# Kernel tuning notes

Hardware: AMD Instinct MI355X
Metric: run time of the kernel (lower is better)

Reference implementation:

```python
import jax, jax.numpy as jnp
import numpy as np

N = 100000
E = 1600000
F = 64
THETA = (0.6, -0.4, 0.3, -0.2, 0.1)  # k = 5 polynomial coefficients


def setup_inputs() -> dict:
    key = jax.random.key(0)
    kx, ke = jax.random.split(key)
    x = jax.random.normal(kx, (N, F), dtype=jnp.float32)
    edge_index = jax.random.randint(ke, (2, E), 0, N, dtype=jnp.int64)
    return {"x": x, "edge_index": edge_index}


def _l_sym_mul(feat, src, dst, deg_inv_sqrt, n):
    # L_sym * feat = feat - D^{-1/2} A D^{-1/2} feat
    src_norm = feat[src] * deg_inv_sqrt[src]            # [E, F] gather + scale
    agg = jax.ops.segment_sum(src_norm, dst, num_segments=n)  # scatter-add to dst
    return feat - deg_inv_sqrt * agg


def reference(x, edge_index):
    src, dst = edge_index[0], edge_index[1]
    n = x.shape[0]
    # in-degree from dst, clamp to >= 1, D^{-1/2} as [N, 1]
    deg = jax.ops.segment_sum(jnp.ones((src.shape[0],), dtype=x.dtype), dst,
                              num_segments=n)
    deg = jnp.maximum(deg, 1.0)[:, None]
    deg_inv_sqrt = deg ** -0.5

    h_acc = THETA[0] * x
    feat = x
    for k in range(1, len(THETA)):
        feat = _l_sym_mul(feat, src, dst, deg_inv_sqrt, n)
        h_acc = h_acc + THETA[k] * feat
    return h_acc
```

## Files before the change

### kernel.cpp

```cpp
#include <hip/hip_runtime.h>


constexpr int kF = 64;
constexpr int BSHIFT = 8;
constexpr int NB = 1 << BSHIFT;
constexpr int TILE = 2048;
constexpr int KMAX = 512;

static __device__ __forceinline__ float bfl(unsigned u) {
    return __uint_as_float(u << 16);
}
static __device__ __forceinline__ float bfh(unsigned u) {
    return __uint_as_float(u & 0xffff0000u);
}
static __device__ __forceinline__ unsigned f2bf(float f) {
    unsigned u = __float_as_uint(f);
    return (u + 0x7fffu + ((u >> 16) & 1u)) >> 16;
}
static __device__ __forceinline__ unsigned pack2(float a, float b) {
    return f2bf(a) | (f2bf(b) << 16);
}

__global__ void k_binA(const int* __restrict__ src, const int* __restrict__ dst,
                       unsigned* __restrict__ pairs, int* __restrict__ gcursor,
                       const float4* __restrict__ x4, uint4* __restrict__ xb4,
                       int n8, int E, int K, int cap) {
    __shared__ int hist[KMAX];
    __shared__ int gb[KMAX];
    const int tid = threadIdx.x;
    const long long tb = (long long)blockIdx.x * TILE;
    const int tcount = (int)min((long long)TILE, (long long)E - tb);

    {
        int per = (n8 + gridDim.x - 1) / (int)gridDim.x;
        int b0 = blockIdx.x * per;
        int b1 = min(b0 + per, n8);
        for (int i = b0 + tid; i < b1; i += 512) {
            float4 a = x4[2 * i];
            float4 b = x4[2 * i + 1];
            uint4 o;
            o.x = pack2(a.x, a.y);
            o.y = pack2(a.z, a.w);
            o.z = pack2(b.x, b.y);
            o.w = pack2(b.z, b.w);
            xb4[i] = o;
        }
    }

    hist[tid] = 0;
    __syncthreads();
    int dc[4], sc[4];
    #pragma unroll
    for (int k = 0; k < 4; ++k) {
        int i = tid + k * 512;
        if (i < tcount) {
            dc[k] = dst[tb + i];
            sc[k] = src[tb + i];
            atomicAdd(&hist[dc[k] >> BSHIFT], 1);
        } else {
            dc[k] = -1;
        }
    }
    __syncthreads();
    int hv = hist[tid];
    gb[tid] = (tid < K && hv > 0) ? atomicAdd(&gcursor[tid], hv) : 0;
    hist[tid] = 0;
    __syncthreads();
    #pragma unroll
    for (int k = 0; k < 4; ++k) {
        if (dc[k] >= 0) {
            int d = dc[k];
            int b = d >> BSHIFT;
            int pos = atomicAdd(&hist[b], 1);
            pairs[(size_t)b * cap + gb[b] + pos] =
                ((unsigned)(d & (NB - 1)) << 23) | (unsigned)sc[k];
        }
    }
}

__global__ void k_binB(const unsigned* __restrict__ pairs, const int* __restrict__ gcursor,
                       int* __restrict__ rp, float* __restrict__ dinv2,
                       float* __restrict__ rdeg, int* __restrict__ csr,
                       const uint4* __restrict__ xb, uint4* __restrict__ g0,
                       int N, int E, int K, int cap) {
    __shared__ int gsc[KMAX];
    __shared__ int cnt[NB];
    __shared__ int stmp[NB];
    __shared__ int cur[NB];
    __shared__ float sdinv[NB];
    const int b = blockIdx.x;
    const int tid = threadIdx.x;

    int gv = (tid < K) ? gcursor[tid] : 0;
    gsc[tid] = gv;
    __syncthreads();
    for (int o = 1; o < KMAX; o <<= 1) {
        int t = (tid >= o) ? gsc[tid - o] : 0;
        __syncthreads();
        gsc[tid] += t;
        __syncthreads();
    }
    const int ecnt = gcursor[b];
    const int base = gsc[b] - ecnt;
    const unsigned* bp = pairs + (size_t)b * cap;

    if (tid < NB) cnt[tid] = 0;
    __syncthreads();
    for (int i = tid; i < ecnt; i += 512)
        atomicAdd(&cnt[bp[i] >> 23], 1);
    __syncthreads();
    int v = (tid < NB) ? cnt[tid] : 0;
    if (tid < NB) stmp[tid] = v;
    __syncthreads();
    for (int o = 1; o < NB; o <<= 1) {
        int t = (tid >= o && tid < NB) ? stmp[tid - o] : 0;
        __syncthreads();
        if (tid < NB) stmp[tid] += t;
        __syncthreads();
    }
    int node = (b << BSHIFT) + tid;
    if (tid < NB) {
        int abs0 = base + stmp[tid] - v;
        cur[tid] = abs0;
        float d = fmaxf((float)v, 1.0f);
        sdinv[tid] = rsqrtf(d);
        if (node < N) {
            rp[node] = abs0;
            dinv2[node] = 1.0f / d;
            rdeg[node]  = sqrtf(d);
        }
    }
    if (b == K - 1 && tid == 0) rp[N] = E;
    __syncthreads();
    for (int i = tid; i < ecnt; i += 512) {
        unsigned p = bp[i];
        int pos = atomicAdd(&cur[p >> 23], 1);
        csr[pos] = (int)(p & 0x7FFFFFu);
    }
    const int nbase = b << BSHIFT;
    const int qmax = min(NB, N - nbase) << 3;
    const uint4* xbp = xb + ((size_t)nbase << 3);
    uint4* g0p = g0 + ((size_t)nbase << 3);
    for (int q = tid; q < qmax; q += 512) {
        float di = sdinv[q >> 3];
        uint4 xv = xbp[q];
        uint4 o;
        o.x = pack2(di * bfl(xv.x), di * bfh(xv.x));
        o.y = pack2(di * bfl(xv.y), di * bfh(xv.y));
        o.z = pack2(di * bfl(xv.z), di * bfh(xv.z));
        o.w = pack2(di * bfl(xv.w), di * bfh(xv.w));
        g0p[q] = o;
    }
}

template <bool LAST>
__global__ void k_gather(const int* __restrict__ rp, const int* __restrict__ csr,
                         const unsigned short* __restrict__ gin,
                         const float* __restrict__ dinv2,
                         unsigned short* __restrict__ gout,
                         const unsigned short* __restrict__ xb,
                         const unsigned short* __restrict__ g1t,
                         const unsigned short* __restrict__ g2t,
                         const float* __restrict__ rdeg,
                         float* __restrict__ h, int n,
                         float t0, float t1, float t2, float t3, float t4) {
    int wid = (blockIdx.x * blockDim.x + threadIdx.x) >> 6;
    int lane = threadIdx.x & 63;
    int half = lane >> 5;
    int r = (lane >> 3) & 3;
    int c = lane & 7;
    int node = wid * 2 + half;
    if (wid * 2 >= n) return;
    bool valid = node < n;
    int beg = valid ? rp[node] : 0;
    int end = valid ? rp[node + 1] : 0;
    int len = end - beg;
    int olen = __shfl_xor(len, 32, 64);
    int mlen = (len > olen) ? len : olen;

    float acc[8] = {0.f, 0.f, 0.f, 0.f, 0.f, 0.f, 0.f, 0.f};

    uint4 rc1 = make_uint4(0, 0, 0, 0), rc2 = make_uint4(0, 0, 0, 0);
    float wc1 = 0.f, wc2 = 0.f;
    int sn1 = 0, sn2 = 0;
    float wn1 = 0.f, wn2 = 0.f;
    if (mlen > 0) {
        int j1 = beg + r, j2 = j1 + 4;
        bool o1 = j1 < end, o2 = j2 < end;
        int s1 = csr[o1 ? j1 : 0];
        int s2 = csr[o2 ? j2 : 0];
        wc1 = o1 ? 1.f : 0.f;
        wc2 = o2 ? 1.f : 0.f;
        rc1 = *(const uint4*)(gin + ((size_t)s1 << 6) + (c << 3));
        rc2 = *(const uint4*)(gin + ((size_t)s2 << 6) + (c << 3));
        int j1b = beg + 8 + r, j2b = j1b + 4;
        bool vb = 8 < mlen;
        bool b1 = vb && (j1b < end), b2 = vb && (j2b < end);
        sn1 = csr[b1 ? j1b : 0];
        sn2 = csr[b2 ? j2b : 0];
        wn1 = b1 ? 1.f : 0.f;
        wn2 = b2 ? 1.f : 0.f;
    }
    for (int i = 0; i < mlen; i += 8) {
        uint4 rn1 = *(const uint4*)(gin + ((size_t)sn1 << 6) + (c << 3));
        uint4 rn2 = *(const uint4*)(gin + ((size_t)sn2 << 6) + (c << 3));
        int j1n = beg + i + 16 + r, j2n = j1n + 4;
        bool vn = (i + 16) < mlen;
        bool t1c = vn && (j1n < end), t2c = vn && (j2n < end);
        int st1 = csr[t1c ? j1n : 0];
        int st2 = csr[t2c ? j2n : 0];
        float wt1 = t1c ? 1.f : 0.f, wt2 = t2c ? 1.f : 0.f;
        acc[0] += wc1 * bfl(rc1.x); acc[1] += wc1 * bfh(rc1.x);
        acc[2] += wc1 * bfl(rc1.y); acc[3] += wc1 * bfh(rc1.y);
        acc[4] += wc1 * bfl(rc1.z); acc[5] += wc1 * bfh(rc1.z);
        acc[6] += wc1 * bfl(rc1.w); acc[7] += wc1 * bfh(rc1.w);
        acc[0] += wc2 * bfl(rc2.x); acc[1] += wc2 * bfh(rc2.x);
        acc[2] += wc2 * bfl(rc2.y); acc[3] += wc2 * bfh(rc2.y);
        acc[4] += wc2 * bfl(rc2.z); acc[5] += wc2 * bfh(rc2.z);
        acc[6] += wc2 * bfl(rc2.w); acc[7] += wc2 * bfh(rc2.w);
        rc1 = rn1; rc2 = rn2;
        wc1 = wn1; wc2 = wn2;
        sn1 = st1; sn2 = st2;
        wn1 = wt1; wn2 = wt2;
    }
    #pragma unroll
    for (int m = 8; m <= 16; m <<= 1) {
        #pragma unroll
        for (int i = 0; i < 8; ++i)
            acc[i] += __shfl_xor(acc[i], m, 64);
    }

    if (r == 0 && valid) {
        size_t off = ((size_t)node << 6) + (c << 3);
        uint4 rr = *(const uint4*)(gin + off);
        float d2 = dinv2[node];
        float v[8];
        v[0] = bfl(rr.x) - d2 * acc[0]; v[1] = bfh(rr.x) - d2 * acc[1];
        v[2] = bfl(rr.y) - d2 * acc[2]; v[3] = bfh(rr.y) - d2 * acc[3];
        v[4] = bfl(rr.z) - d2 * acc[4]; v[5] = bfh(rr.z) - d2 * acc[5];
        v[6] = bfl(rr.w) - d2 * acc[6]; v[7] = bfh(rr.w) - d2 * acc[7];
        if (!LAST) {
            uint4 o;
            o.x = pack2(v[0], v[1]);
            o.y = pack2(v[2], v[3]);
            o.z = pack2(v[4], v[5]);
            o.w = pack2(v[6], v[7]);
            *(uint4*)(gout + off) = o;
        } else {
            uint4 xv = *(const uint4*)(xb + off);
            uint4 a  = *(const uint4*)(g1t + off);
            uint4 b  = *(const uint4*)(g2t + off);
            float rd = rdeg[node];
            float s1 = rd * t1, s2 = rd * t2, s3 = rd * t3, s4 = rd * t4;
            float4 h0, h1;
            h0.x = t0 * bfl(xv.x) + s1 * bfl(a.x) + s2 * bfl(b.x) + s3 * bfl(rr.x) + s4 * v[0];
            h0.y = t0 * bfh(xv.x) + s1 * bfh(a.x) + s2 * bfh(b.x) + s3 * bfh(rr.x) + s4 * v[1];
            h0.z = t0 * bfl(xv.y) + s1 * bfl(a.y) + s2 * bfl(b.y) + s3 * bfl(rr.y) + s4 * v[2];
            h0.w = t0 * bfh(xv.y) + s1 * bfh(a.y) + s2 * bfh(b.y) + s3 * bfh(rr.y) + s4 * v[3];
            h1.x = t0 * bfl(xv.z) + s1 * bfl(a.z) + s2 * bfl(b.z) + s3 * bfl(rr.z) + s4 * v[4];
            h1.y = t0 * bfh(xv.z) + s1 * bfh(a.z) + s2 * bfh(b.z) + s3 * bfh(rr.z) + s4 * v[5];
            h1.z = t0 * bfl(xv.w) + s1 * bfl(a.w) + s2 * bfl(b.w) + s3 * bfl(rr.w) + s4 * v[6];
            h1.w = t0 * bfh(xv.w) + s1 * bfh(a.w) + s2 * bfh(b.w) + s3 * bfh(rr.w) + s4 * v[7];
            *(float4*)(h + off) = h0;
            *(float4*)(h + off + 4) = h1;
        }
    }
}

extern "C" void kernel_launch(void* const* d_in, const int* in_sizes, int n_in,
                              void* d_out, int out_size, void* d_ws, size_t ws_size,
                              hipStream_t stream) {
    const float* x  = (const float*)d_in[0];
    const int*   ei = (const int*)d_in[1];
    const int N = in_sizes[0] / kF;
    const int E = in_sizes[1] / 2;
    const int* src = ei;
    const int* dst = ei + E;
    float* h = (float*)d_out;

    const int K = (N + NB - 1) >> BSHIFT;
    const int cap = 2 * ((E + K - 1) / K);

    char* ws = (char*)d_ws;
    size_t off = 0;
    auto carve = [&](size_t bytes) {
        void* p = ws + off;
        off = (off + bytes + 511) & ~(size_t)511;
        return p;
    };
    int*            gcursor = (int*)carve((size_t)K * 4);
    int*            rp      = (int*)carve((size_t)(N + 1) * 4);
    float*          dinv2   = (float*)carve((size_t)N * 4);
    float*          rdeg    = (float*)carve((size_t)N * 4);
    int*            csr     = (int*)carve((size_t)E * 4);
    unsigned short* xb      = (unsigned short*)carve((size_t)N * kF * 2);
    unsigned short* g0      = (unsigned short*)carve((size_t)N * kF * 2);
    unsigned short* g1      = (unsigned short*)carve((size_t)N * kF * 2);
    unsigned short* g2      = (unsigned short*)carve((size_t)N * kF * 2);
    size_t gbytes = (size_t)N * kF * 2;
    size_t pbytes = (size_t)K * cap * 4;
    unsigned short* g3      = (unsigned short*)carve(gbytes > pbytes ? gbytes : pbytes);
    unsigned*       pairs   = (unsigned*)g3;

    const float theta[5] = {0.6f, -0.4f, 0.3f, -0.2f, 0.1f};
    const int n8 = N * kF / 8;

    hipMemsetAsync(gcursor, 0, (size_t)K * 4, stream);
    k_binA<<<(E + TILE - 1) / TILE, 512, 0, stream>>>(src, dst, pairs, gcursor,
                                                      (const float4*)x, (uint4*)xb,
                                                      n8, E, K, cap);
    k_binB<<<K, 512, 0, stream>>>(pairs, gcursor, rp, dinv2, rdeg, csr,
                                  (const uint4*)xb, (uint4*)g0, N, E, K, cap);

    const int nwaves = (N + 1) / 2;
    const int gblocks = (nwaves + 3) / 4;
    k_gather<false><<<gblocks, 256, 0, stream>>>(rp, csr, g0, dinv2, g1,
                                                 nullptr, nullptr, nullptr, nullptr,
                                                 nullptr, N, 0, 0, 0, 0, 0);
    k_gather<false><<<gblocks, 256, 0, stream>>>(rp, csr, g1, dinv2, g2,
                                                 nullptr, nullptr, nullptr, nullptr,
                                                 nullptr, N, 0, 0, 0, 0, 0);
    k_gather<false><<<gblocks, 256, 0, stream>>>(rp, csr, g2, dinv2, g3,
                                                 nullptr, nullptr, nullptr, nullptr,
                                                 nullptr, N, 0, 0, 0, 0, 0);
    k_gather<true><<<gblocks, 256, 0, stream>>>(rp, csr, g3, dinv2, nullptr,
                                                xb, g1, g2, rdeg, h, N,
                                                theta[0], theta[1], theta[2],
                                                theta[3], theta[4]);
}
```

Baseline: 248.3 us.

## Split bf16 features into four 16-wide chunk planes to shrink gather working set

Stores the bf16 feature buffers as four planes of 16 features each (32 bytes per node). Each gather launch now covers all four chunks, with blocks grouped by chunk so that concurrently running blocks touch a smaller random-access set that fits better in cache. Each wave now handles 16 edges per step with 2 lanes per node row, and intermediate stores and final loads use nontemporal hints. The trade-off is that the CSR indices are read four times, and each random row fetch is only 32 bytes.

Result: slower. 442.2 us (+78.1%).

```diff
diff --git a/kernel.cpp b/kernel.cpp
--- a/kernel.cpp
+++ b/kernel.cpp
@@ -2,10 +2,15 @@
 
 
 constexpr int kF = 64;
+constexpr int CH = 4;
+constexpr int CF = 16;
 constexpr int BSHIFT = 8;
 constexpr int NB = 1 << BSHIFT;
 constexpr int TILE = 2048;
 constexpr int KMAX = 512;
+
+typedef unsigned nv4u __attribute__((ext_vector_type(4)));
+typedef float    nv4f __attribute__((ext_vector_type(4)));
 
 static __device__ __forceinline__ float bfl(unsigned u) {
     return __uint_as_float(u << 16);
@@ -30,6 +35,7 @@
     const int tid = threadIdx.x;
     const long long tb = (long long)blockIdx.x * TILE;
     const int tcount = (int)min((long long)TILE, (long long)E - tb);
+    const int Nn = n8 >> 3;
 
     {
         int per = (n8 + gridDim.x - 1) / (int)gridDim.x;
@@ -43,7 +49,9 @@
             o.y = pack2(a.z, a.w);
             o.z = pack2(b.x, b.y);
             o.w = pack2(b.z, b.w);
-            xb4[i] = o;
+            int nloc = i >> 3, sub = i & 7;
+            int c = sub >> 1, dd = sub & 1;
+            xb4[(size_t)c * ((size_t)Nn * 2) + (size_t)nloc * 2 + dd] = o;
         }
     }
 
@@ -81,7 +89,7 @@
 __global__ void k_binB(const unsigned* __restrict__ pairs, const int* __restrict__ gcursor,
                        int* __restrict__ rp, float* __restrict__ dinv2,
                        float* __restrict__ rdeg, int* __restrict__ csr,
-                       const uint4* __restrict__ xb, uint4* __restrict__ g0,
+                       const uint4* __restrict__ xb4, uint4* __restrict__ g04,
                        int N, int E, int K, int cap) {
     __shared__ int gsc[KMAX];
     __shared__ int cnt[NB];
@@ -138,18 +146,20 @@
         csr[pos] = (int)(p & 0x7FFFFFu);
     }
     const int nbase = b << BSHIFT;
-    const int qmax = min(NB, N - nbase) << 3;
-    const uint4* xbp = xb + ((size_t)nbase << 3);
-    uint4* g0p = g0 + ((size_t)nbase << 3);
-    for (int q = tid; q < qmax; q += 512) {
-        float di = sdinv[q >> 3];
-        uint4 xv = xbp[q];
-        uint4 o;
-        o.x = pack2(di * bfl(xv.x), di * bfh(xv.x));
-        o.y = pack2(di * bfl(xv.y), di * bfh(xv.y));
-        o.z = pack2(di * bfl(xv.z), di * bfh(xv.z));
-        o.w = pack2(di * bfl(xv.w), di * bfh(xv.w));
-        g0p[q] = o;
+    const int nn = min(NB, N - nbase);
+    for (int c = 0; c < CH; ++c) {
+        const uint4* xp = xb4 + (size_t)c * ((size_t)N * 2) + (size_t)nbase * 2;
+        uint4*       gp = g04 + (size_t)c * ((size_t)N * 2) + (size_t)nbase * 2;
+        for (int q = tid; q < nn * 2; q += 512) {
+            float di = sdinv[q >> 1];
+            uint4 xv = xp[q];
+            uint4 o;
+            o.x = pack2(di * bfl(xv.x), di * bfh(xv.x));
+            o.y = pack2(di * bfl(xv.y), di * bfh(xv.y));
+            o.z = pack2(di * bfl(xv.z), di * bfh(xv.z));
+            o.w = pack2(di * bfl(xv.w), di * bfh(xv.w));
+            gp[q] = o;
+        }
     }
 }
 
@@ -162,14 +172,16 @@
                          const unsigned short* __restrict__ g1t,
                          const unsigned short* __restrict__ g2t,
                          const float* __restrict__ rdeg,
-                         float* __restrict__ h, int n,
+                         float* __restrict__ h, int n, int cblocks,
                          float t0, float t1, float t2, float t3, float t4) {
-    int wid = (blockIdx.x * blockDim.x + threadIdx.x) >> 6;
-    int lane = threadIdx.x & 63;
-    int half = lane >> 5;
-    int r = (lane >> 3) & 3;
-    int c = lane & 7;
-    int node = wid * 2 + half;
+    const int chunk = blockIdx.x / cblocks;
+    const int bidx  = blockIdx.x - chunk * cblocks;
+    const int wid   = bidx * 4 + (threadIdx.x >> 6);
+    const int lane  = threadIdx.x & 63;
+    const int half  = lane >> 5;
+    const int e     = (lane >> 1) & 15;
+    const int d     = lane & 1;
+    const int node  = wid * 2 + half;
     if (wid * 2 >= n) return;
     bool valid = node < n;
     int beg = valid ? rp[node] : 0;
@@ -178,60 +190,46 @@
     int olen = __shfl_xor(len, 32, 64);
     int mlen = (len > olen) ? len : olen;
 
+    const unsigned short* gp = gin + (size_t)chunk * ((size_t)n * CF);
+
     float acc[8] = {0.f, 0.f, 0.f, 0.f, 0.f, 0.f, 0.f, 0.f};
 
-    uint4 rc1 = make_uint4(0, 0, 0, 0), rc2 = make_uint4(0, 0, 0, 0);
-    float wc1 = 0.f, wc2 = 0.f;
-    int sn1 = 0, sn2 = 0;
-    float wn1 = 0.f, wn2 = 0.f;
+    uint4 rc = make_uint4(0, 0, 0, 0);
+    float wc = 0.f, wn = 0.f;
+    int sn = 0;
     if (mlen > 0) {
-        int j1 = beg + r, j2 = j1 + 4;
-        bool o1 = j1 < end, o2 = j2 < end;
-        int s1 = csr[o1 ? j1 : 0];
-        int s2 = csr[o2 ? j2 : 0];
-        wc1 = o1 ? 1.f : 0.f;
-        wc2 = o2 ? 1.f : 0.f;
-        rc1 = *(const uint4*)(gin + ((size_t)s1 << 6) + (c << 3));
-        rc2 = *(const uint4*)(gin + ((size_t)s2 << 6) + (c << 3));
-        int j1b = beg + 8 + r, j2b = j1b + 4;
-        bool vb = 8 < mlen;
-        bool b1 = vb && (j1b < end), b2 = vb && (j2b < end);
-        sn1 = csr[b1 ? j1b : 0];
-        sn2 = csr[b2 ? j2b : 0];
-        wn1 = b1 ? 1.f : 0.f;
-        wn2 = b2 ? 1.f : 0.f;
-    }
-    for (int i = 0; i < mlen; i += 8) {
-        uint4 rn1 = *(const uint4*)(gin + ((size_t)sn1 << 6) + (c << 3));
-        uint4 rn2 = *(const uint4*)(gin + ((size_t)sn2 << 6) + (c << 3));
-        int j1n = beg + i + 16 + r, j2n = j1n + 4;
-        bool vn = (i + 16) < mlen;
-        bool t1c = vn && (j1n < end), t2c = vn && (j2n < end);
-        int st1 = csr[t1c ? j1n : 0];
-        int st2 = csr[t2c ? j2n : 0];
-        float wt1 = t1c ? 1.f : 0.f, wt2 = t2c ? 1.f : 0.f;
-        acc[0] += wc1 * bfl(rc1.x); acc[1] += wc1 * bfh(rc1.x);
-        acc[2] += wc1 * bfl(rc1.y); acc[3] += wc1 * bfh(rc1.y);
-        acc[4] += wc1 * bfl(rc1.z); acc[5] += wc1 * bfh(rc1.z);
-        acc[6] += wc1 * bfl(rc1.w); acc[7] += wc1 * bfh(rc1.w);
-        acc[0] += wc2 * bfl(rc2.x); acc[1] += wc2 * bfh(rc2.x);
-        acc[2] += wc2 * bfl(rc2.y); acc[3] += wc2 * bfh(rc2.y);
-        acc[4] += wc2 * bfl(rc2.z); acc[5] += wc2 * bfh(rc2.z);
-        acc[6] += wc2 * bfl(rc2.w); acc[7] += wc2 * bfh(rc2.w);
-        rc1 = rn1; rc2 = rn2;
-        wc1 = wn1; wc2 = wn2;
-        sn1 = st1; sn2 = st2;
-        wn1 = wt1; wn2 = wt2;
+        int j = beg + e;
+        bool o = j < end;
+        int s = csr[o ? j : 0];
+        wc = o ? 1.f : 0.f;
+        rc = *(const uint4*)(gp + (size_t)s * CF + (d << 3));
+        int jb = beg + 16 + e;
+        bool bnext = (16 < mlen) && (jb < end);
+        sn = csr[bnext ? jb : 0];
+        wn = bnext ? 1.f : 0.f;
+    }
+    for (int i = 0; i < mlen; i += 16) {
+        uint4 rn = *(const uint4*)(gp + (size_t)sn * CF + (d << 3));
+        int jn = beg + i + 32 + e;
+        bool tn = ((i + 32) < mlen) && (jn < end);
+        int st = csr[tn ? jn : 0];
+        float wt = tn ? 1.f : 0.f;
+        acc[0] += wc * bfl(rc.x); acc[1] += wc * bfh(rc.x);
+        acc[2] += wc * bfl(rc.y); acc[3] += wc * bfh(rc.y);
+        acc[4] += wc * bfl(rc.z); acc[5] += wc * bfh(rc.z);
+        acc[6] += wc * bfl(rc.w); acc[7] += wc * bfh(rc.w);
+        rc = rn; wc = wn;
+        sn = st; wn = wt;
     }
     #pragma unroll
-    for (int m = 8; m <= 16; m <<= 1) {
+    for (int m = 2; m <= 16; m <<= 1) {
         #pragma unroll
         for (int i = 0; i < 8; ++i)
             acc[i] += __shfl_xor(acc[i], m, 64);
     }
 
-    if (r == 0 && valid) {
-        size_t off = ((size_t)node << 6) + (c << 3);
+    if (e == 0 && valid) {
+        size_t off = (size_t)chunk * ((size_t)n * CF) + (size_t)node * CF + (d << 3);
         uint4 rr = *(const uint4*)(gin + off);
         float d2 = dinv2[node];
         float v[8];
@@ -240,19 +238,19 @@
         v[4] = bfl(rr.z) - d2 * acc[4]; v[5] = bfh(rr.z) - d2 * acc[5];
         v[6] = bfl(rr.w) - d2 * acc[6]; v[7] = bfh(rr.w) - d2 * acc[7];
         if (!LAST) {
-            uint4 o;
+            nv4u o;
             o.x = pack2(v[0], v[1]);
             o.y = pack2(v[2], v[3]);
             o.z = pack2(v[4], v[5]);
             o.w = pack2(v[6], v[7]);
-            *(uint4*)(gout + off) = o;
+            __builtin_nontemporal_store(o, (nv4u*)(gout + off));
         } else {
-            uint4 xv = *(const uint4*)(xb + off);
-            uint4 a  = *(const uint4*)(g1t + off);
-            uint4 b  = *(const uint4*)(g2t + off);
+            nv4u xv = __builtin_nontemporal_load((const nv4u*)(xb + off));
+            nv4u a  = __builtin_nontemporal_load((const nv4u*)(g1t + off));
+            nv4u b  = __builtin_nontemporal_load((const nv4u*)(g2t + off));
             float rd = rdeg[node];
             float s1 = rd * t1, s2 = rd * t2, s3 = rd * t3, s4 = rd * t4;
-            float4 h0, h1;
+            nv4f h0, h1;
             h0.x = t0 * bfl(xv.x) + s1 * bfl(a.x) + s2 * bfl(b.x) + s3 * bfl(rr.x) + s4 * v[0];
             h0.y = t0 * bfh(xv.x) + s1 * bfh(a.x) + s2 * bfh(b.x) + s3 * bfh(rr.x) + s4 * v[1];
             h0.z = t0 * bfl(xv.y) + s1 * bfl(a.y) + s2 * bfl(b.y) + s3 * bfl(rr.y) + s4 * v[2];
@@ -261,8 +259,9 @@
             h1.y = t0 * bfh(xv.z) + s1 * bfh(a.z) + s2 * bfh(b.z) + s3 * bfh(rr.z) + s4 * v[5];
             h1.z = t0 * bfl(xv.w) + s1 * bfl(a.w) + s2 * bfl(b.w) + s3 * bfl(rr.w) + s4 * v[6];
             h1.w = t0 * bfh(xv.w) + s1 * bfh(a.w) + s2 * bfh(b.w) + s3 * bfh(rr.w) + s4 * v[7];
-            *(float4*)(h + off) = h0;
-            *(float4*)(h + off + 4) = h1;
+            size_t hoff = (size_t)node * kF + chunk * CF + (d << 3);
+            __builtin_nontemporal_store(h0, (nv4f*)(h + hoff));
+            __builtin_nontemporal_store(h1, (nv4f*)(h + hoff + 4));
         }
     }
 }
@@ -313,18 +312,20 @@
                                   (const uint4*)xb, (uint4*)g0, N, E, K, cap);
 
     const int nwaves = (N + 1) / 2;
-    const int gblocks = (nwaves + 3) / 4;
+    int cblocks = (nwaves + 3) / 4;
+    cblocks = (cblocks + 7) & ~7;
+    const int gblocks = CH * cblocks;
     k_gather<false><<<gblocks, 256, 0, stream>>>(rp, csr, g0, dinv2, g1,
                                                  nullptr, nullptr, nullptr, nullptr,
-                                                 nullptr, N, 0, 0, 0, 0, 0);
+                                                 nullptr, N, cblocks, 0, 0, 0, 0, 0);
     k_gather<false><<<gblocks, 256, 0, stream>>>(rp, csr, g1, dinv2, g2,
                                                  nullptr, nullptr, nullptr, nullptr,
-                                                 nullptr, N, 0, 0, 0, 0, 0);
+                                                 nullptr, N, cblocks, 0, 0, 0, 0, 0);
     k_gather<false><<<gblocks, 256, 0, stream>>>(rp, csr, g2, dinv2, g3,
                                                  nullptr, nullptr, nullptr, nullptr,
-                                                 nullptr, N, 0, 0, 0, 0, 0);
+                                                 nullptr, N, cblocks, 0, 0, 0, 0, 0);
     k_gather<true><<<gblocks, 256, 0, stream>>>(rp, csr, g3, dinv2, nullptr,
-                                                xb, g1, g2, rdeg, h, N,
+                                                xb, g1, g2, rdeg, h, N, cblocks,
                                                 theta[0], theta[1], theta[2],
                                                 theta[3], theta[4]);
 }
```

## Switch intermediates to fp16 with packed half2 accumulation and zero sentinel row

Applied to the files above, without the earlier changes.

Intermediate feature buffers move from bf16 to fp16, and neighbour accumulation now uses packed half2 adds instead of per-element fp32 FMAs with 0/1 weights. Invalid neighbour slots are redirected to a zeroed sentinel row at index N, so the weight multiplies are no longer needed. Final-stage loads and stores become nontemporal, and the workspace layout is reshuffled so the pairs buffer aliases g1. The half2 accumulation lowers ALU and register cost but risks fp16 overflow and precision loss on high-degree sums.

Result: no change. 244.5 us (-1.5%).

```diff
diff --git a/kernel.cpp b/kernel.cpp
--- a/kernel.cpp
+++ b/kernel.cpp
@@ -1,4 +1,5 @@
 #include <hip/hip_runtime.h>
+#include <hip/hip_fp16.h>
 
 
 constexpr int kF = 64;
@@ -7,18 +8,24 @@
 constexpr int TILE = 2048;
 constexpr int KMAX = 512;
 
-static __device__ __forceinline__ float bfl(unsigned u) {
-    return __uint_as_float(u << 16);
-}
-static __device__ __forceinline__ float bfh(unsigned u) {
-    return __uint_as_float(u & 0xffff0000u);
-}
-static __device__ __forceinline__ unsigned f2bf(float f) {
-    unsigned u = __float_as_uint(f);
-    return (u + 0x7fffu + ((u >> 16) & 1u)) >> 16;
-}
-static __device__ __forceinline__ unsigned pack2(float a, float b) {
-    return f2bf(a) | (f2bf(b) << 16);
+typedef unsigned nv4u __attribute__((ext_vector_type(4)));
+typedef float    nv4f __attribute__((ext_vector_type(4)));
+
+static __device__ __forceinline__ float hlo(unsigned u) {
+    return __half2float(__ushort_as_half((unsigned short)(u & 0xffffu)));
+}
+static __device__ __forceinline__ float hhi(unsigned u) {
+    return __half2float(__ushort_as_half((unsigned short)(u >> 16)));
+}
+static __device__ __forceinline__ unsigned pack2h(float a, float b) {
+    return (unsigned)__half_as_ushort(__float2half_rn(a)) |
+           ((unsigned)__half_as_ushort(__float2half_rn(b)) << 16);
+}
+static __device__ __forceinline__ unsigned padd2(unsigned a, unsigned b) {
+    __half2 ha = *reinterpret_cast<__half2*>(&a);
+    __half2 hb = *reinterpret_cast<__half2*>(&b);
+    __half2 hc = __hadd2(ha, hb);
+    return *reinterpret_cast<unsigned*>(&hc);
 }
 
 __global__ void k_binA(const int* __restrict__ src, const int* __restrict__ dst,
@@ -39,10 +46,10 @@
             float4 a = x4[2 * i];
             float4 b = x4[2 * i + 1];
             uint4 o;
-            o.x = pack2(a.x, a.y);
-            o.y = pack2(a.z, a.w);
-            o.z = pack2(b.x, b.y);
-            o.w = pack2(b.z, b.w);
+            o.x = pack2h(a.x, a.y);
+            o.y = pack2h(a.z, a.w);
+            o.z = pack2h(b.x, b.y);
+            o.w = pack2h(b.z, b.w);
             xb4[i] = o;
         }
     }
@@ -91,6 +98,9 @@
     const int b = blockIdx.x;
     const int tid = threadIdx.x;
 
+    if (b == 0 && tid < 8)
+        g0[((size_t)N << 3) + tid] = make_uint4(0, 0, 0, 0);
+
     int gv = (tid < K) ? gcursor[tid] : 0;
     gsc[tid] = gv;
     __syncthreads();
@@ -145,10 +155,10 @@
         float di = sdinv[q >> 3];
         uint4 xv = xbp[q];
         uint4 o;
-        o.x = pack2(di * bfl(xv.x), di * bfh(xv.x));
-        o.y = pack2(di * bfl(xv.y), di * bfh(xv.y));
-        o.z = pack2(di * bfl(xv.z), di * bfh(xv.z));
-        o.w = pack2(di * bfl(xv.w), di * bfh(xv.w));
+        o.x = pack2h(di * hlo(xv.x), di * hhi(xv.x));
+        o.y = pack2h(di * hlo(xv.y), di * hhi(xv.y));
+        o.z = pack2h(di * hlo(xv.z), di * hhi(xv.z));
+        o.w = pack2h(di * hlo(xv.w), di * hhi(xv.w));
         g0p[q] = o;
     }
 }
@@ -164,6 +174,9 @@
                          const float* __restrict__ rdeg,
                          float* __restrict__ h, int n,
                          float t0, float t1, float t2, float t3, float t4) {
+    if (!LAST && blockIdx.x == 0 && threadIdx.x < 8)
+        *(((uint4*)(gout + ((size_t)n << 6))) + threadIdx.x) = make_uint4(0, 0, 0, 0);
+
     int wid = (blockIdx.x * blockDim.x + threadIdx.x) >> 6;
     int lane = threadIdx.x & 63;
     int half = lane >> 5;
@@ -178,28 +191,22 @@
     int olen = __shfl_xor(len, 32, 64);
     int mlen = (len > olen) ? len : olen;
 
-    float acc[8] = {0.f, 0.f, 0.f, 0.f, 0.f, 0.f, 0.f, 0.f};
+    unsigned acc[4] = {0u, 0u, 0u, 0u};
 
     uint4 rc1 = make_uint4(0, 0, 0, 0), rc2 = make_uint4(0, 0, 0, 0);
-    float wc1 = 0.f, wc2 = 0.f;
-    int sn1 = 0, sn2 = 0;
-    float wn1 = 0.f, wn2 = 0.f;
+    int sn1 = n, sn2 = n;
     if (mlen > 0) {
         int j1 = beg + r, j2 = j1 + 4;
         bool o1 = j1 < end, o2 = j2 < end;
-        int s1 = csr[o1 ? j1 : 0];
-        int s2 = csr[o2 ? j2 : 0];
-        wc1 = o1 ? 1.f : 0.f;
-        wc2 = o2 ? 1.f : 0.f;
+        int s1 = csr[o1 ? j1 : 0]; s1 = o1 ? s1 : n;
+        int s2 = csr[o2 ? j2 : 0]; s2 = o2 ? s2 : n;
         rc1 = *(const uint4*)(gin + ((size_t)s1 << 6) + (c << 3));
         rc2 = *(const uint4*)(gin + ((size_t)s2 << 6) + (c << 3));
         int j1b = beg + 8 + r, j2b = j1b + 4;
         bool vb = 8 < mlen;
         bool b1 = vb && (j1b < end), b2 = vb && (j2b < end);
-        sn1 = csr[b1 ? j1b : 0];
-        sn2 = csr[b2 ? j2b : 0];
-        wn1 = b1 ? 1.f : 0.f;
-        wn2 = b2 ? 1.f : 0.f;
+        sn1 = csr[b1 ? j1b : 0]; sn1 = b1 ? sn1 : n;
+        sn2 = csr[b2 ? j2b : 0]; sn2 = b2 ? sn2 : n;
     }
     for (int i = 0; i < mlen; i += 8) {
         uint4 rn1 = *(const uint4*)(gin + ((size_t)sn1 << 6) + (c << 3));
@@ -207,27 +214,20 @@
         int j1n = beg + i + 16 + r, j2n = j1n + 4;
         bool vn = (i + 16) < mlen;
         bool t1c = vn && (j1n < end), t2c = vn && (j2n < end);
-        int st1 = csr[t1c ? j1n : 0];
-        int st2 = csr[t2c ? j2n : 0];
-        float wt1 = t1c ? 1.f : 0.f, wt2 = t2c ? 1.f : 0.f;
-        acc[0] += wc1 * bfl(rc1.x); acc[1] += wc1 * bfh(rc1.x);
-        acc[2] += wc1 * bfl(rc1.y); acc[3] += wc1 * bfh(rc1.y);
-        acc[4] += wc1 * bfl(rc1.z); acc[5] += wc1 * bfh(rc1.z);
-        acc[6] += wc1 * bfl(rc1.w); acc[7] += wc1 * bfh(rc1.w);
-        acc[0] += wc2 * bfl(rc2.x); acc[1] += wc2 * bfh(rc2.x);
-        acc[2] += wc2 * bfl(rc2.y); acc[3] += wc2 * bfh(rc2.y);
-        acc[4] += wc2 * bfl(rc2.z); acc[5] += wc2 * bfh(rc2.z);
-        acc[6] += wc2 * bfl(rc2.w); acc[7] += wc2 * bfh(rc2.w);
+        int st1 = csr[t1c ? j1n : 0]; st1 = t1c ? st1 : n;
+        int st2 = csr[t2c ? j2n : 0]; st2 = t2c ? st2 : n;
+        acc[0] = padd2(acc[0], rc1.x); acc[1] = padd2(acc[1], rc1.y);
+        acc[2] = padd2(acc[2], rc1.z); acc[3] = padd2(acc[3], rc1.w);
+        acc[0] = padd2(acc[0], rc2.x); acc[1] = padd2(acc[1], rc2.y);
+        acc[2] = padd2(acc[2], rc2.z); acc[3] = padd2(acc[3], rc2.w);
         rc1 = rn1; rc2 = rn2;
-        wc1 = wn1; wc2 = wn2;
         sn1 = st1; sn2 = st2;
-        wn1 = wt1; wn2 = wt2;
     }
     #pragma unroll
     for (int m = 8; m <= 16; m <<= 1) {
         #pragma unroll
-        for (int i = 0; i < 8; ++i)
-            acc[i] += __shfl_xor(acc[i], m, 64);
+        for (int i = 0; i < 4; ++i)
+            acc[i] = padd2(acc[i], __shfl_xor(acc[i], m, 64));
     }
 
     if (r == 0 && valid) {
@@ -235,34 +235,34 @@
         uint4 rr = *(const uint4*)(gin + off);
         float d2 = dinv2[node];
         float v[8];
-        v[0] = bfl(rr.x) - d2 * acc[0]; v[1] = bfh(rr.x) - d2 * acc[1];
-        v[2] = bfl(rr.y) - d2 * acc[2]; v[3] = bfh(rr.y) - d2 * acc[3];
-        v[4] = bfl(rr.z) - d2 * acc[4]; v[5] = bfh(rr.z) - d2 * acc[5];
-        v[6] = bfl(rr.w) - d2 * acc[6]; v[7] = bfh(rr.w) - d2 * acc[7];
+        v[0] = hlo(rr.x) - d2 * hlo(acc[0]); v[1] = hhi(rr.x) - d2 * hhi(acc[0]);
+        v[2] = hlo(rr.y) - d2 * hlo(acc[1]); v[3] = hhi(rr.y) - d2 * hhi(acc[1]);
+        v[4] = hlo(rr.z) - d2 * hlo(acc[2]); v[5] = hhi(rr.z) - d2 * hhi(acc[2]);
+        v[6] = hlo(rr.w) - d2 * hlo(acc[3]); v[7] = hhi(rr.w) - d2 * hhi(acc[3]);
         if (!LAST) {
-            uint4 o;
-            o.x = pack2(v[0], v[1]);
-            o.y = pack2(v[2], v[3]);
-            o.z = pack2(v[4], v[5]);
-            o.w = pack2(v[6], v[7]);
-            *(uint4*)(gout + off) = o;
+            nv4u o;
+            o.x = pack2h(v[0], v[1]);
+            o.y = pack2h(v[2], v[3]);
+            o.z = pack2h(v[4], v[5]);
+            o.w = pack2h(v[6], v[7]);
+            __builtin_nontemporal_store(o, (nv4u*)(gout + off));
         } else {
-            uint4 xv = *(const uint4*)(xb + off);
-            uint4 a  = *(const uint4*)(g1t + off);
-            uint4 b  = *(const uint4*)(g2t + off);
+            nv4u xv = __builtin_nontemporal_load((const nv4u*)(xb + off));
+            nv4u a  = __builtin_nontemporal_load((const nv4u*)(g1t + off));
+            nv4u b  = __builtin_nontemporal_load((const nv4u*)(g2t + off));
             float rd = rdeg[node];
             float s1 = rd * t1, s2 = rd * t2, s3 = rd * t3, s4 = rd * t4;
-            float4 h0, h1;
-            h0.x = t0 * bfl(xv.x) + s1 * bfl(a.x) + s2 * bfl(b.x) + s3 * bfl(rr.x) + s4 * v[0];
-            h0.y = t0 * bfh(xv.x) + s1 * bfh(a.x) + s2 * bfh(b.x) + s3 * bfh(rr.x) + s4 * v[1];
-            h0.z = t0 * bfl(xv.y) + s1 * bfl(a.y) + s2 * bfl(b.y) + s3 * bfl(rr.y) + s4 * v[2];
-            h0.w = t0 * bfh(xv.y) + s1 * bfh(a.y) + s2 * bfh(b.y) + s3 * bfh(rr.y) + s4 * v[3];
-            h1.x = t0 * bfl(xv.z) + s1 * bfl(a.z) + s2 * bfl(b.z) + s3 * bfl(rr.z) + s4 * v[4];
-            h1.y = t0 * bfh(xv.z) + s1 * bfh(a.z) + s2 * bfh(b.z) + s3 * bfh(rr.z) + s4 * v[5];
-            h1.z = t0 * bfl(xv.w) + s1 * bfl(a.w) + s2 * bfl(b.w) + s3 * bfl(rr.w) + s4 * v[6];
-            h1.w = t0 * bfh(xv.w) + s1 * bfh(a.w) + s2 * bfh(b.w) + s3 * bfh(rr.w) + s4 * v[7];
-            *(float4*)(h + off) = h0;
-            *(float4*)(h + off + 4) = h1;
+            nv4f h0, h1;
+            h0.x = t0 * hlo(xv.x) + s1 * hlo(a.x) + s2 * hlo(b.x) + s3 * hlo(rr.x) + s4 * v[0];
+            h0.y = t0 * hhi(xv.x) + s1 * hhi(a.x) + s2 * hhi(b.x) + s3 * hhi(rr.x) + s4 * v[1];
+            h0.z = t0 * hlo(xv.y) + s1 * hlo(a.y) + s2 * hlo(b.y) + s3 * hlo(rr.y) + s4 * v[2];
+            h0.w = t0 * hhi(xv.y) + s1 * hhi(a.y) + s2 * hhi(b.y) + s3 * hhi(rr.y) + s4 * v[3];
+            h1.x = t0 * hlo(xv.z) + s1 * hlo(a.z) + s2 * hlo(b.z) + s3 * hlo(rr.z) + s4 * v[4];
+            h1.y = t0 * hhi(xv.z) + s1 * hhi(a.z) + s2 * hhi(b.z) + s3 * hhi(rr.z) + s4 * v[5];
+            h1.z = t0 * hlo(xv.w) + s1 * hlo(a.w) + s2 * hlo(b.w) + s3 * hlo(rr.w) + s4 * v[6];
+            h1.w = t0 * hhi(xv.w) + s1 * hhi(a.w) + s2 * hhi(b.w) + s3 * hhi(rr.w) + s4 * v[7];
+            __builtin_nontemporal_store(h0, (nv4f*)(h + off));
+            __builtin_nontemporal_store(h1, (nv4f*)(h + off + 4));
         }
     }
 }
@@ -288,19 +288,19 @@
         off = (off + bytes + 511) & ~(size_t)511;
         return p;
     };
+    size_t gbytes = (size_t)(N + 1) * kF * 2;
     int*            gcursor = (int*)carve((size_t)K * 4);
     int*            rp      = (int*)carve((size_t)(N + 1) * 4);
     float*          dinv2   = (float*)carve((size_t)N * 4);
     float*          rdeg    = (float*)carve((size_t)N * 4);
     int*            csr     = (int*)carve((size_t)E * 4);
     unsigned short* xb      = (unsigned short*)carve((size_t)N * kF * 2);
-    unsigned short* g0      = (unsigned short*)carve((size_t)N * kF * 2);
-    unsigned short* g1      = (unsigned short*)carve((size_t)N * kF * 2);
-    unsigned short* g2      = (unsigned short*)carve((size_t)N * kF * 2);
-    size_t gbytes = (size_t)N * kF * 2;
+    unsigned short* g0      = (unsigned short*)carve(gbytes);
     size_t pbytes = (size_t)K * cap * 4;
-    unsigned short* g3      = (unsigned short*)carve(gbytes > pbytes ? gbytes : pbytes);
-    unsigned*       pairs   = (unsigned*)g3;
+    unsigned short* g1      = (unsigned short*)carve(gbytes > pbytes ? gbytes : pbytes);
+    unsigned short* g2      = (unsigned short*)carve(gbytes);
+    unsigned short* g3      = (unsigned short*)carve(gbytes);
+    unsigned*       pairs   = (unsigned*)g1;
 
     const float theta[5] = {0.6f, -0.4f, 0.3f, -0.2f, 0.1f};
     const int n8 = N * kF / 8;
```
